# Performance work log

Hardware: AMD Instinct MI355X
Metric: run time of the kernel (lower is better)

## Reference

```python
import jax, jax.numpy as jnp
import numpy as np

B, S, E, G, O, TOPK = 4, 2048, 1024, 8, 4096, 2


def setup_inputs() -> dict:
    key = jax.random.key(0)
    k1, k2, k3, k4 = jax.random.split(key, 4)
    return {
        "hidden_states": jax.random.normal(k1, (B, S, E), dtype=jnp.float32),
        "WG": jax.random.normal(k2, (E, G), dtype=jnp.float32) * (1.0 / np.sqrt(E)),
        "Wi": jax.random.normal(k3, (G, E, O), dtype=jnp.float32) * (1.0 / np.sqrt(E)),
        "down": jax.random.normal(k4, (O, E), dtype=jnp.float32) * (1.0 / np.sqrt(O)),
        "topk": TOPK,
    }


def reference(hidden_states, WG, Wi, down, topk):
    # gate logits: [b, s, g]
    gate = jnp.matmul(hidden_states, WG)
    # sparse path (smoe_fwd): topk mask zeroes non-selected gate LOGITS,
    # so non-selected experts get sigmoid(0) = 0.5 (faithful to source).
    _, idx = jax.lax.top_k(gate, topk)              # [b, s, topk]
    mask = jnp.max(jax.nn.one_hot(idx, gate.shape[-1], dtype=gate.dtype), axis=-2)  # [b, s, g]
    w = jax.nn.sigmoid(gate * mask)                  # [b, s, g]
    # weighted combination over all expert matrices: [b, s, o]
    y = jnp.einsum('bse,bsg,geo->bso', hidden_states, w, Wi)
    # squared ReLU
    h = jnp.square(jax.nn.relu(y))
    return jnp.matmul(h, down)                       # [b, s, e]
```

## Files before the change

### kernel.cpp

```cpp
#include <hip/hip_runtime.h>
#include <hip/hip_bf16.h>
#include <math.h>

typedef __bf16 bf16;
typedef __bf16 bf16x4 __attribute__((ext_vector_type(4)));
typedef __bf16 bf16x8 __attribute__((ext_vector_type(8)));
typedef float  floatx4 __attribute__((ext_vector_type(4)));

#define N_TOK 8192
#define E_DIM 1024
#define G_DIM 8
#define O_DIM 4096
#define EPI_LD 132

__device__ __forceinline__ void gload_lds16(const void* g, void* l) {
    __builtin_amdgcn_global_load_lds(
        (__attribute__((address_space(1))) void*)(g),
        (__attribute__((address_space(3))) void*)(l),
        16, 0, 0);
}

__global__ __launch_bounds__(256) void gate_compute(
    const float* __restrict__ X,
    const float* __restrict__ WG,
    int* __restrict__ sel,
    float* __restrict__ sval,
    bf16* __restrict__ Xb)
{
    __shared__ float lwgT[G_DIM * E_DIM];
    const int tid  = threadIdx.x;
    const int wave = tid >> 6;
    const int lane = tid & 63;

#pragma unroll
    for (int k = 0; k < 8; ++k) {
        const int i = k * 256 + tid;
        const float4 v = *(const float4*)(WG + i * 4);
        const int e  = i >> 1;
        const int g0 = (i & 1) * 4;
        lwgT[(g0 + 0) * E_DIM + e] = v.x;
        lwgT[(g0 + 1) * E_DIM + e] = v.y;
        lwgT[(g0 + 2) * E_DIM + e] = v.z;
        lwgT[(g0 + 3) * E_DIM + e] = v.w;
    }
    __syncthreads();

    const int t = blockIdx.x * 4 + wave;
    float acc[G_DIM];
#pragma unroll
    for (int g = 0; g < G_DIM; ++g) acc[g] = 0.f;

#pragma unroll
    for (int it = 0; it < 4; ++it) {
        const int e0 = it * 256 + lane * 4;
        const float4 xv = *(const float4*)(X + (long)t * E_DIM + e0);
        bf16x4 xo;
        xo[0] = (bf16)xv.x; xo[1] = (bf16)xv.y;
        xo[2] = (bf16)xv.z; xo[3] = (bf16)xv.w;
        *(bf16x4*)(Xb + (long)t * E_DIM + e0) = xo;
#pragma unroll
        for (int g = 0; g < G_DIM; ++g) {
            const float4 wv = *(const float4*)(lwgT + g * E_DIM + e0);
            acc[g] += xv.x * wv.x + xv.y * wv.y + xv.z * wv.z + xv.w * wv.w;
        }
    }
#pragma unroll
    for (int g = 0; g < G_DIM; ++g) {
        float v = acc[g];
#pragma unroll
        for (int off = 32; off > 0; off >>= 1) v += __shfl_down(v, off, 64);
        acc[g] = v;
    }
    if (lane == 0) {
        int i1 = 0;
#pragma unroll
        for (int g = 1; g < G_DIM; ++g) if (acc[g] > acc[i1]) i1 = g;
        int i2 = (i1 == 0) ? 1 : 0;
#pragma unroll
        for (int g = 0; g < G_DIM; ++g)
            if (g != i1 && g != i2 && acc[g] > acc[i2]) i2 = g;
#pragma unroll
        for (int s = 0; s < 2; ++s) {
            const int g = s ? i2 : i1;
            sel[t * 2 + s]  = g;
            sval[t * 2 + s] = 1.f / (1.f + expf(-acc[g])) - 0.5f;
        }
    }
}

__global__ __launch_bounds__(1024) void route_kernel(
    const int* __restrict__ sel, const float* __restrict__ sval,
    int* __restrict__ cnt, int* __restrict__ off, int* __restrict__ offp,
    int* __restrict__ tok, float* __restrict__ scl, int* __restrict__ pos)
{
    __shared__ int hcnt[16][G_DIM];
    __shared__ int wbase[16][G_DIM];
    const int tid  = threadIdx.x;
    const int w    = tid >> 6;
    const int lane = tid & 63;
    const unsigned long long below = ((unsigned long long)1 << lane) - 1;

    int c0[G_DIM];
#pragma unroll
    for (int g = 0; g < G_DIM; ++g) c0[g] = 0;
    for (int c = 0; c < 16; ++c) {
        const int g = sel[w * 1024 + c * 64 + lane];
#pragma unroll
        for (int gg = 0; gg < G_DIM; ++gg)
            c0[gg] += __popcll(__ballot(g == gg));
    }
    if (lane == 0)
#pragma unroll
        for (int g = 0; g < G_DIM; ++g) hcnt[w][g] = c0[g];
    __syncthreads();

    if (tid == 0) {
        int tot[G_DIM];
#pragma unroll
        for (int g = 0; g < G_DIM; ++g) {
            int a = 0;
            for (int ww = 0; ww < 16; ++ww) { wbase[ww][g] = a; a += hcnt[ww][g]; }
            tot[g] = a; cnt[g] = a;
        }
        int a = 0, b = 0;
#pragma unroll
        for (int g = 0; g < G_DIM; ++g) {
            off[g]  = a; a += tot[g];
            offp[g] = b; b += (tot[g] + 127) & ~127;
        }
        offp[G_DIM] = b;
    }
    __syncthreads();

    int run[G_DIM];
#pragma unroll
    for (int g = 0; g < G_DIM; ++g) run[g] = 0;
    for (int c = 0; c < 16; ++c) {
        const int idx = w * 1024 + c * 64 + lane;
        const int g   = sel[idx];
        const float sv = sval[idx];
        int myrank = 0;
#pragma unroll
        for (int gg = 0; gg < G_DIM; ++gg) {
            const unsigned long long m = __ballot(g == gg);
            const int r = run[gg] + __popcll(m & below);
            if (g == gg) myrank = r;
            run[gg] += __popcll(m);
        }
        const int p = wbase[w][g] + myrank;
        tok[g * N_TOK + p] = idx >> 1;
        scl[g * N_TOK + p] = sv;
        pos[idx] = (g << 16) | p;
    }
}

__global__ __launch_bounds__(256) void transpose_conv(
    const float* __restrict__ S, bf16* __restrict__ D, int R, int C)
{
    __shared__ float tile[64][65];
    const int r0  = blockIdx.x * 64;
    const int c0  = blockIdx.y * 64;
    const int tid = threadIdx.x;
    const int tr  = tid >> 4;
    const int tc4 = (tid & 15) * 4;

#pragma unroll
    for (int p = 0; p < 4; ++p) {
        const int r = p * 16 + tr;
        const float4 v = *(const float4*)(S + (long)(r0 + r) * C + c0 + tc4);
        tile[r][tc4 + 0] = v.x;
        tile[r][tc4 + 1] = v.y;
        tile[r][tc4 + 2] = v.z;
        tile[r][tc4 + 3] = v.w;
    }
    __syncthreads();
#pragma unroll
    for (int p = 0; p < 4; ++p) {
        const int c = p * 16 + tr;
        bf16x4 o;
        o[0] = (bf16)tile[tc4 + 0][c];
        o[1] = (bf16)tile[tc4 + 1][c];
        o[2] = (bf16)tile[tc4 + 2][c];
        o[3] = (bf16)tile[tc4 + 3][c];
        *(bf16x4*)(D + (long)(c0 + c) * R + r0 + tc4) = o;
    }
}

__global__ __launch_bounds__(256) void transpose_wi_wsum(
    const float* __restrict__ Wi,
    bf16* __restrict__ WiT,
    bf16* __restrict__ WsumT)
{
    __shared__ float tile[64][65];
    const int e0  = blockIdx.x * 64;
    const int c0  = blockIdx.y * 64;
    const int tid = threadIdx.x;
    const int tr  = tid >> 4;
    const int tc4 = (tid & 15) * 4;

    float acc[4][4] = {};

    for (int g = 0; g < G_DIM; ++g) {
        __syncthreads();
#pragma unroll
        for (int p = 0; p < 4; ++p) {
            const int r = p * 16 + tr;
            const float4 v = *(const float4*)(
                Wi + (long)(g * 1024 + e0 + r) * O_DIM + c0 + tc4);
            tile[r][tc4 + 0] = v.x;
            tile[r][tc4 + 1] = v.y;
            tile[r][tc4 + 2] = v.z;
            tile[r][tc4 + 3] = v.w;
        }
        __syncthreads();
#pragma unroll
        for (int p = 0; p < 4; ++p) {
            const int c = p * 16 + tr;
            bf16x4 o;
#pragma unroll
            for (int k = 0; k < 4; ++k) {
                const float f = tile[tc4 + k][c];
                o[k] = (bf16)f;
                acc[p][k] += f;
            }
            *(bf16x4*)(WiT + (long)(c0 + c) * 8192 + g * 1024 + e0 + tc4) = o;
        }
    }
#pragma unroll
    for (int p = 0; p < 4; ++p) {
        const int c = p * 16 + tr;
        bf16x4 w;
#pragma unroll
        for (int k = 0; k < 4; ++k) w[k] = (bf16)(0.5f * acc[p][k]);
        *(bf16x4*)(WsumT + (long)(c0 + c) * E_DIM + e0 + tc4) = w;
    }
}

__global__ __launch_bounds__(512) void gather_rows(
    const bf16* __restrict__ Xb, const int* __restrict__ cnt,
    const int* __restrict__ offp, const int* __restrict__ tok,
    bf16* __restrict__ Xs)
{
    const int slot = blockIdx.x * 4 + (threadIdx.x >> 7);
    const int l    = threadIdx.x & 127;
    if (slot >= offp[G_DIM]) return;
    int g = 0;
    while (slot >= offp[g + 1]) ++g;
    const int p = slot - offp[g];
    bf16* dst = Xs + (long)slot * E_DIM + l * 8;
    if (p < cnt[g]) {
        const bf16* src = Xb + (long)tok[g * N_TOK + p] * E_DIM + l * 8;
        *(bf16x8*)dst = *(const bf16x8*)src;
    } else {
        bf16x8 z = {};
        *(bf16x8*)dst = z;
    }
}

__device__ __forceinline__ void gemm_core256(
    const bf16* __restrict__ Ap, long lda,
    const bf16* __restrict__ Bp, long ldb,
    int K, char* smem, floatx4 (&acc)[8][4])
{
    const int tid  = threadIdx.x;
    const int wave = tid >> 6;
    const int lane = tid & 63;
    const int wm   = wave >> 2;
    const int wn   = wave & 3;
    const int fr   = lane & 15;
    const int fq   = lane >> 4;

#pragma unroll
    for (int i = 0; i < 8; ++i)
#pragma unroll
        for (int j = 0; j < 4; ++j)
            acc[i][j] = (floatx4){0.f, 0.f, 0.f, 0.f};

    const int  srow = tid >> 2;
    const int  ksw  = (((tid & 3) ^ ((tid >> 3) & 3)) << 4);
    const char* sa  = (const char*)Ap + (long)srow * (lda * 2) + ksw;
    const char* sb  = (const char*)Bp + (long)srow * (ldb * 2) + ksw;
    const long aR   = lda * 256;
    const long bR   = ldb * 256;
    const int  ldsW = wave * 1024;

#define STAGE_H(sbase, src, rstr, kb) do {                                   \
        gload_lds16((src) + (kb),          smem + (sbase) + ldsW);           \
        gload_lds16((src) + (kb) + (rstr), smem + (sbase) + 8192 + ldsW);    \
    } while (0)

    const int asw = ((fq ^ ((fr >> 1) & 3)) << 4);
    const int aro = (wm * 128 + fr) * 64 + asw;
    const int bro = (wn * 64 + fr) * 64 + asw;

    const int nt = K >> 6;

    {
        const long k1 = (nt > 1) ? 128 : 0;
        STAGE_H(0,             sa, aR, 0);
        STAGE_H(32768,         sb, bR, 0);
        STAGE_H(16384,         sa, aR, 64);
        STAGE_H(49152,         sb, bR, 64);
        STAGE_H(65536 + 32768, sb, bR, k1);
        STAGE_H(65536 + 0,     sa, aR, k1);
    }
    asm volatile("s_waitcnt vmcnt(4)" ::: "memory");
    __builtin_amdgcn_s_barrier();

#define LD8(v, off) (v) = *(const bf16x8*)(smem + (off))
#define PHASE_MID()   __builtin_amdgcn_s_barrier()
#define PHASE_END()   __builtin_amdgcn_s_barrier()
#define PHASE_END_V() do {                                                   \
        asm volatile("s_waitcnt vmcnt(8)" ::: "memory");                     \
        __builtin_amdgcn_s_barrier();                                        \
    } while (0)

    bf16x8 af[4], bq[4];

    for (int t = 0; t < nt; ++t) {
        const int  bo  = (t & 1) << 16;
        const int  nbo = bo ^ 65536;
        const long k1  = (long)((t + 1 < nt) ? t + 1 : nt - 1) * 128;
        const long k2  = (long)((t + 2 < nt) ? t + 2 : nt - 1) * 128;

#pragma unroll
        for (int i = 0; i < 4; ++i) LD8(af[i], bo + aro + i * 1024);
#pragma unroll
        for (int j = 0; j < 4; ++j) LD8(bq[j], bo + 32768 + bro + j * 1024);
        STAGE_H(nbo + 49152, sb, bR, k1 + 64);
        PHASE_MID();
        __builtin_amdgcn_s_setprio(1);
#pragma unroll
        for (int i = 0; i < 4; ++i)
#pragma unroll
            for (int j = 0; j < 4; ++j)
                acc[i][j] = __builtin_amdgcn_mfma_f32_16x16x32_bf16(
                    af[i], bq[j], acc[i][j], 0, 0, 0);
        __builtin_amdgcn_s_setprio(0);
        PHASE_END();

#pragma unroll
        for (int i = 0; i < 4; ++i) LD8(af[i], bo + aro + 4096 + i * 1024);
        STAGE_H(nbo + 16384, sa, aR, k1 + 64);
        PHASE_MID();
        __builtin_amdgcn_s_setprio(1);
#pragma unroll
        for (int i = 0; i < 4; ++i)
#pragma unroll
            for (int j = 0; j < 4; ++j)
                acc[4 + i][j] = __builtin_amdgcn_mfma_f32_16x16x32_bf16(
                    af[i], bq[j], acc[4 + i][j], 0, 0, 0);
        __builtin_amdgcn_s_setprio(0);
        PHASE_END_V();

#pragma unroll
        for (int i = 0; i < 4; ++i) LD8(af[i], bo + 16384 + aro + i * 1024);
#pragma unroll
        for (int j = 0; j < 4; ++j) LD8(bq[j], bo + 49152 + bro + j * 1024);
        STAGE_H(bo + 32768, sb, bR, k2);
        PHASE_MID();
        __builtin_amdgcn_s_setprio(1);
#pragma unroll
        for (int i = 0; i < 4; ++i)
#pragma unroll
            for (int j = 0; j < 4; ++j)
                acc[i][j] = __builtin_amdgcn_mfma_f32_16x16x32_bf16(
                    af[i], bq[j], acc[i][j], 0, 0, 0);
        __builtin_amdgcn_s_setprio(0);
        PHASE_END();

#pragma unroll
        for (int i = 0; i < 4; ++i) LD8(af[i], bo + 16384 + aro + 4096 + i * 1024);
        STAGE_H(bo + 0, sa, aR, k2);
        PHASE_MID();
        __builtin_amdgcn_s_setprio(1);
#pragma unroll
        for (int i = 0; i < 4; ++i)
#pragma unroll
            for (int j = 0; j < 4; ++j)
                acc[4 + i][j] = __builtin_amdgcn_mfma_f32_16x16x32_bf16(
                    af[i], bq[j], acc[4 + i][j], 0, 0, 0);
        __builtin_amdgcn_s_setprio(0);
        PHASE_END_V();
    }

    asm volatile("s_waitcnt vmcnt(0)" ::: "memory");
    __builtin_amdgcn_s_barrier();
#undef STAGE_H
#undef LD8
#undef PHASE_MID
#undef PHASE_END
#undef PHASE_END_V
}

__global__ __launch_bounds__(512, 2) void gemm256_base(
    const bf16* __restrict__ A, const bf16* __restrict__ BT,
    bf16* __restrict__ C)
{
    __shared__ __align__(16) char smem[131072];
    const int u   = blockIdx.x;
    const int xcd = u & 7;
    const int s   = u >> 3;
    const int mt  = s & 31;
    const int ct  = xcd + 8 * (s >> 5);
    const int row0 = mt * 256, col0 = ct * 256;

    floatx4 acc[8][4];
    gemm_core256(A + (long)row0 * E_DIM, E_DIM,
                 BT + (long)col0 * E_DIM, E_DIM,
                 E_DIM, smem, acc);

    const int tid = threadIdx.x, wave = tid >> 6, lane = tid & 63;
    const int wm = wave >> 2, wn = wave & 3, fr = lane & 15, fq = lane >> 4;
    bf16* tile = (bf16*)smem;
#pragma unroll
    for (int i = 0; i < 8; ++i)
#pragma unroll
        for (int j = 0; j < 4; ++j)
#pragma unroll
            for (int r = 0; r < 4; ++r)
                tile[(wm * 128 + i * 16 + fq * 4 + r) * 256 + wn * 64 + j * 16 + fr] =
                    (bf16)(acc[i][j][r]);
    __syncthreads();
#pragma unroll
    for (int k = 0; k < 16; ++k) {
        const int rl = (tid >> 5) + k * 16;
        const int cc = (tid & 31) * 8;
        *(bf16x8*)(C + (long)(row0 + rl) * O_DIM + col0 + cc) =
            *(const bf16x8*)(tile + rl * 256 + cc);
    }
}

__global__ __launch_bounds__(512, 2) void gemm256_sparse(
    const bf16* __restrict__ Xs,
    const bf16* __restrict__ WiT,
    const int* __restrict__ cnt,
    const int* __restrict__ off,
    const int* __restrict__ offp,
    const float* __restrict__ scl,
    bf16* __restrict__ ysp)
{
    const int u   = blockIdx.x;
    const int xcd = u & 7;
    const int s   = u >> 3;
    const int mt  = s & 63;
    const int pc  = xcd + 8 * (s >> 6);
    const int g   = pc & 7;
    const int ct  = pc >> 3;

    const int cg     = cnt[g];
    const int base_p = offp[g];
    const int cgp    = offp[g + 1] - base_p;
    const int m0     = mt * 256;
    if (m0 >= cgp) return;

    __shared__ __align__(16) char smem[131072];
    const int col0 = ct * 256;

    floatx4 acc[8][4];
    gemm_core256(Xs + (long)(base_p + m0) * E_DIM, E_DIM,
                 WiT + (long)col0 * 8192 + g * E_DIM, 8192,
                 E_DIM, smem, acc);

    const int tid = threadIdx.x, wave = tid >> 6, lane = tid & 63;
    const int wm = wave >> 2, wn = wave & 3, fr = lane & 15, fq = lane >> 4;
    const float* sclg = scl + g * N_TOK;
    const int clmax = cg - 1;
    bf16* tile = (bf16*)smem;
#pragma unroll
    for (int i = 0; i < 8; ++i)
#pragma unroll
        for (int r = 0; r < 4; ++r) {
            const int rl = wm * 128 + i * 16 + fq * 4 + r;
            const int gm = m0 + rl;
            const float sv = sclg[gm > clmax ? clmax : gm];
#pragma unroll
            for (int j = 0; j < 4; ++j)
                tile[rl * 256 + wn * 64 + j * 16 + fr] = (bf16)(sv * acc[i][j][r]);
        }
    __syncthreads();
    const long ob = off[g] + m0;
#pragma unroll
    for (int k = 0; k < 16; ++k) {
        const int rl = (tid >> 5) + k * 16;
        if (m0 + rl < cg) {
            const int cc = (tid & 31) * 8;
            *(bf16x8*)(ysp + (ob + rl) * O_DIM + col0 + cc) =
                *(const bf16x8*)(tile + rl * 256 + cc);
        }
    }
}

template <typename OUT, bool VEC>
__global__ __launch_bounds__(256, 4) void gemm_mt(
    const bf16* __restrict__ A, int lda,
    const bf16* __restrict__ BT, int ldb,
    OUT* __restrict__ C, int ldc, int K)
{
    __shared__ char smem[VEC ? (128 * EPI_LD * 2) : 16384];
    bf16* As = (bf16*)smem;
    bf16* Bs = (bf16*)(smem + 8192);

    const int u   = blockIdx.x;
    const int xcd = u & 7;
    const int s   = u >> 3;
    const int mt  = s & 63;
    const int col = xcd + 8 * (s >> 6);

    const int tid  = threadIdx.x;
    const int wave = tid >> 6;
    const int lane = tid & 63;
    const int row0 = mt * 128;
    const int col0 = col * 128;

    const int sr = lane >> 2;
    const int sc = (lane & 3) * 8;
    const bf16* agp0 = A  + (long)(row0 + 16 * wave       + sr) * lda + sc;
    const bf16* agp1 = A  + (long)(row0 + 16 * (wave + 4) + sr) * lda + sc;
    const bf16* bgp0 = BT + (long)(col0 + 16 * wave       + sr) * ldb + sc;
    const bf16* bgp1 = BT + (long)(col0 + 16 * (wave + 4) + sr) * ldb + sc;
    bf16* asl0 = As + (long)wave * 512;
    bf16* asl1 = As + (long)(wave + 4) * 512;
    bf16* bsl0 = Bs + (long)wave * 512;
    bf16* bsl1 = Bs + (long)(wave + 4) * 512;

    const int mi_base = (wave >> 1) * 64;
    const int ni_base = (wave & 1) * 64;
    const int fr = lane & 15;
    const int fq = lane >> 4;

    floatx4 acc[4][4] = {};

    for (int k0 = 0; k0 < K; k0 += 32) {
        __syncthreads();
        gload_lds16(agp0 + k0, (void*)asl0);
        gload_lds16(agp1 + k0, (void*)asl1);
        gload_lds16(bgp0 + k0, (void*)bsl0);
        gload_lds16(bgp1 + k0, (void*)bsl1);
        __syncthreads();

        bf16x8 af[4], bfr[4];
#pragma unroll
        for (int i = 0; i < 4; ++i) {
            af[i]  = *(const bf16x8*)(As + (mi_base + i * 16 + fr) * 32 + fq * 8);
            bfr[i] = *(const bf16x8*)(Bs + (ni_base + i * 16 + fr) * 32 + fq * 8);
        }
#pragma unroll
        for (int i = 0; i < 4; ++i)
#pragma unroll
            for (int j = 0; j < 4; ++j)
                acc[i][j] = __builtin_amdgcn_mfma_f32_16x16x32_bf16(
                    af[i], bfr[j], acc[i][j], 0, 0, 0);
    }

    if (VEC) {
        __syncthreads();
        bf16* tile = (bf16*)smem;
#pragma unroll
        for (int i = 0; i < 4; ++i)
#pragma unroll
            for (int j = 0; j < 4; ++j)
#pragma unroll
                for (int r = 0; r < 4; ++r) {
                    const int rl = mi_base + i * 16 + fq * 4 + r;
                    const int cl = ni_base + j * 16 + fr;
                    tile[rl * EPI_LD + cl] = (bf16)acc[i][j][r];
                }
        __syncthreads();
#pragma unroll
        for (int k = 0; k < 8; ++k) {
            const int rl = (tid >> 3) + 32 * (k >> 1);
            const int cl = (tid & 7) * 8 + 64 * (k & 1);
            const bf16x8 v = *(const bf16x8*)(tile + rl * EPI_LD + cl);
            *(bf16x8*)((bf16*)C + (long)(row0 + rl) * ldc + col0 + cl) = v;
        }
    } else {
#pragma unroll
        for (int i = 0; i < 4; ++i)
#pragma unroll
            for (int j = 0; j < 4; ++j)
#pragma unroll
                for (int r = 0; r < 4; ++r) {
                    const long row = row0 + mi_base + i * 16 + fq * 4 + r;
                    const long cg  = col0 + ni_base + j * 16 + fr;
                    C[row * ldc + cg] = (OUT)acc[i][j][r];
                }
    }
}

__global__ __launch_bounds__(512) void relu2_gather(
    const bf16* __restrict__ Yb,
    const bf16* __restrict__ ysp,
    const int* __restrict__ pos,
    const int* __restrict__ off,
    bf16* __restrict__ H)
{
    const int t  = blockIdx.x * 2 + (threadIdx.x >> 8);
    const int p0 = pos[t * 2];
    const int p1 = pos[t * 2 + 1];
    const long r0 = off[p0 >> 16] + (p0 & 0xffff);
    const long r1 = off[p1 >> 16] + (p1 & 0xffff);
    const int c = (threadIdx.x & 255) * 16;

    const bf16* yb = Yb + (long)t * O_DIM + c;
    const bf16* s0 = ysp + r0 * O_DIM + c;
    const bf16* s1 = ysp + r1 * O_DIM + c;
    bf16* hp = H + (long)t * O_DIM + c;

#pragma unroll
    for (int h = 0; h < 2; ++h) {
        const bf16x8 a = *(const bf16x8*)(yb + h * 8);
        const bf16x8 b = *(const bf16x8*)(s0 + h * 8);
        const bf16x8 d = *(const bf16x8*)(s1 + h * 8);
        bf16x8 o;
#pragma unroll
        for (int k = 0; k < 8; ++k) {
            float v = (float)a[k] + (float)b[k] + (float)d[k];
            v = fmaxf(v, 0.f);
            o[k] = (bf16)(v * v);
        }
        *(bf16x8*)(hp + h * 8) = o;
    }
}

extern "C" void kernel_launch(void* const* d_in, const int* in_sizes, int n_in,
                              void* d_out, int out_size, void* d_ws, size_t ws_size,
                              hipStream_t stream)
{
    const float* X  = (const float*)d_in[0];
    const float* WG = (const float*)d_in[1];
    const float* Wi = (const float*)d_in[2];
    const float* dn = (const float*)d_in[3];
    float* out = (float*)d_out;

    char* ws = (char*)d_ws;
    const long MB = 1l << 20;
    int*   cnt   = (int*)ws;
    int*   off   = (int*)(ws + 1024);
    int*   offp  = (int*)(ws + 2048);
    int*   pos   = (int*)(ws + 4096);
    int*   tok   = (int*)(ws + 128 * 1024);
    float* scl   = (float*)(ws + 448 * 1024);
    int*   sel   = (int*)(ws + 704 * 1024);
    float* sval  = (float*)(ws + 768 * 1024);
    bf16*  dnT   = (bf16*)(ws + 1 * MB);
    bf16*  WiT   = (bf16*)(ws + 9 * MB);
    bf16*  Hh    = (bf16*)(ws + 9 * MB);
    bf16*  Xs    = (bf16*)(ws + 73 * MB);
    bf16*  Yb    = (bf16*)(ws + 107 * MB);
    bf16*  ysp   = (bf16*)(ws + 171 * MB);
    bf16*  Xb    = (bf16*)(ws + 171 * MB);
    bf16*  WsumT = (bf16*)(ws + 187 * MB);

    gate_compute<<<dim3(N_TOK / 4), dim3(256), 0, stream>>>(X, WG, sel, sval, Xb);
    route_kernel<<<dim3(1), dim3(1024), 0, stream>>>(sel, sval, cnt, off, offp,
                                                     tok, scl, pos);
    transpose_wi_wsum<<<dim3(E_DIM / 64, O_DIM / 64), dim3(256), 0, stream>>>(
        Wi, WiT, WsumT);
    transpose_conv<<<dim3(O_DIM / 64, E_DIM / 64), dim3(256), 0, stream>>>(dn, dnT, O_DIM, E_DIM);
    gemm256_base<<<dim3(512), dim3(512), 0, stream>>>(Xb, WsumT, Yb);
    gather_rows<<<dim3(17408 / 4), dim3(512), 0, stream>>>(Xb, cnt, offp, tok, Xs);
    gemm256_sparse<<<dim3(8192), dim3(512), 0, stream>>>(
        Xs, WiT, cnt, off, offp, scl, ysp);
    relu2_gather<<<dim3(N_TOK / 2), dim3(512), 0, stream>>>(Yb, ysp, pos, off, Hh);
    gemm_mt<float, false><<<dim3(64 * 8), dim3(256), 0, stream>>>(
        Hh, O_DIM, dnT, O_DIM, out, E_DIM, O_DIM);
}
```

Before: 722.9 us.

## Split sparse expert GEMM into per-expert-pair launches and stage down-proj output

The sparse expert GEMM is now issued as four launches, each covering two experts, instead of one launch spanning all eight. The block-to-tile mapping changes so that each XCD's blocks work within a single expert pair, which should keep that expert's weight columns hot in L2. The final down-projection GEMM, which wrote scattered scalar floats, now stages its results through LDS in two row halves and writes coalesced float4 stores. The cost is three extra kernel launches, possible tail idling between launches, and a larger LDS footprint for the down GEMM.

```diff
diff --git a/kernel.cpp b/kernel.cpp
--- a/kernel.cpp
+++ b/kernel.cpp
@@ -11,7 +11,6 @@
 #define E_DIM 1024
 #define G_DIM 8
 #define O_DIM 4096
-#define EPI_LD 132
 
 __device__ __forceinline__ void gload_lds16(const void* g, void* l) {
     __builtin_amdgcn_global_load_lds(
@@ -438,15 +437,16 @@
     const int* __restrict__ off,
     const int* __restrict__ offp,
     const float* __restrict__ scl,
-    bf16* __restrict__ ysp)
+    bf16* __restrict__ ysp,
+    int gpair)
 {
     const int u   = blockIdx.x;
     const int xcd = u & 7;
     const int s   = u >> 3;
     const int mt  = s & 63;
     const int pc  = xcd + 8 * (s >> 6);
-    const int g   = pc & 7;
-    const int ct  = pc >> 3;
+    const int g   = gpair * 2 + (pc & 1);
+    const int ct  = pc >> 1;
 
     const int cg     = cnt[g];
     const int base_p = offp[g];
@@ -491,13 +491,12 @@
     }
 }
 
-template <typename OUT, bool VEC>
-__global__ __launch_bounds__(256, 4) void gemm_mt(
+__global__ __launch_bounds__(256, 4) void gemm_down(
     const bf16* __restrict__ A, int lda,
     const bf16* __restrict__ BT, int ldb,
-    OUT* __restrict__ C, int ldc, int K)
-{
-    __shared__ char smem[VEC ? (128 * EPI_LD * 2) : 16384];
+    float* __restrict__ C, int ldc, int K)
+{
+    __shared__ __align__(16) char smem[33792];
     bf16* As = (bf16*)smem;
     bf16* Bs = (bf16*)(smem + 8192);
 
@@ -553,38 +552,28 @@
                     af[i], bfr[j], acc[i][j], 0, 0, 0);
     }
 
-    if (VEC) {
+    float* ftile = (float*)smem;
+#pragma unroll
+    for (int p = 0; p < 2; ++p) {
         __syncthreads();
-        bf16* tile = (bf16*)smem;
-#pragma unroll
-        for (int i = 0; i < 4; ++i)
-#pragma unroll
-            for (int j = 0; j < 4; ++j)
-#pragma unroll
-                for (int r = 0; r < 4; ++r) {
-                    const int rl = mi_base + i * 16 + fq * 4 + r;
-                    const int cl = ni_base + j * 16 + fr;
-                    tile[rl * EPI_LD + cl] = (bf16)acc[i][j][r];
-                }
+        if ((mi_base >> 6) == p) {
+#pragma unroll
+            for (int i = 0; i < 4; ++i)
+#pragma unroll
+                for (int j = 0; j < 4; ++j)
+#pragma unroll
+                    for (int r = 0; r < 4; ++r)
+                        ftile[(i * 16 + fq * 4 + r) * 132 + ni_base + j * 16 + fr]
+                            = acc[i][j][r];
+        }
         __syncthreads();
+        const int rl = tid >> 2;
 #pragma unroll
         for (int k = 0; k < 8; ++k) {
-            const int rl = (tid >> 3) + 32 * (k >> 1);
-            const int cl = (tid & 7) * 8 + 64 * (k & 1);
-            const bf16x8 v = *(const bf16x8*)(tile + rl * EPI_LD + cl);
-            *(bf16x8*)((bf16*)C + (long)(row0 + rl) * ldc + col0 + cl) = v;
-        }
-    } else {
-#pragma unroll
-        for (int i = 0; i < 4; ++i)
-#pragma unroll
-            for (int j = 0; j < 4; ++j)
-#pragma unroll
-                for (int r = 0; r < 4; ++r) {
-                    const long row = row0 + mi_base + i * 16 + fq * 4 + r;
-                    const long cg  = col0 + ni_base + j * 16 + fr;
-                    C[row * ldc + cg] = (OUT)acc[i][j][r];
-                }
+            const int cf = (tid & 3) + 4 * k;
+            const float4 v = *(const float4*)&ftile[rl * 132 + cf * 4];
+            *(float4*)(C + (long)(row0 + p * 64 + rl) * ldc + col0 + cf * 4) = v;
+        }
     }
 }
 
@@ -660,9 +649,10 @@
     transpose_conv<<<dim3(O_DIM / 64, E_DIM / 64), dim3(256), 0, stream>>>(dn, dnT, O_DIM, E_DIM);
     gemm256_base<<<dim3(512), dim3(512), 0, stream>>>(Xb, WsumT, Yb);
     gather_rows<<<dim3(17408 / 4), dim3(512), 0, stream>>>(Xb, cnt, offp, tok, Xs);
-    gemm256_sparse<<<dim3(8192), dim3(512), 0, stream>>>(
-        Xs, WiT, cnt, off, offp, scl, ysp);
+    for (int gp = 0; gp < 4; ++gp)
+        gemm256_sparse<<<dim3(2048), dim3(512), 0, stream>>>(
+            Xs, WiT, cnt, off, offp, scl, ysp, gp);
     relu2_gather<<<dim3(N_TOK / 2), dim3(512), 0, stream>>>(Yb, ysp, pos, off, Hh);
-    gemm_mt<float, false><<<dim3(64 * 8), dim3(256), 0, stream>>>(
+    gemm_down<<<dim3(64 * 8), dim3(256), 0, stream>>>(
         Hh, O_DIM, dnT, O_DIM, out, E_DIM, O_DIM);
 }
```

Result: slower. 752.4 us (+4.1%).
